# Optimization experiments

Measured on AMD Instinct MI355X. Metric: run time of the kernel, lower is better.

## Reference

```python
import jax, jax.numpy as jnp
import numpy as np


def setup_inputs() -> dict:
    key = jax.random.key(0)
    kq, kk, kv = jax.random.split(key, 3)
    B, S, D = 4, 4096, 128
    return {
        "q_proj": jax.random.normal(kq, (B, S, D), dtype=jnp.float32),
        "k_proj": jax.random.normal(kk, (B, S, D), dtype=jnp.float32),
        "v_proj": jax.random.normal(kv, (B, S, D), dtype=jnp.float32),
    }


def reference(q_proj, k_proj, v_proj):
    # Block-wise online softmax in the original is mathematically exact
    # full (non-causal) scaled dot-product attention.
    d = q_proj.shape[-1]
    scale = 1.0 / jnp.sqrt(jnp.asarray(d, dtype=q_proj.dtype))
    logits = jnp.einsum('bqd,bkd->bqk', q_proj, k_proj) * scale  # [B,S,S]
    attn = jax.nn.softmax(logits, axis=-1)
    return jnp.einsum('bqk,bkd->bqd', attn, v_proj)
```

## Files before the change

### kernel.cpp

```cpp
#include <hip/hip_runtime.h>
#include <hip/hip_bf16.h>
#include <stdint.h>

#define Bn 4
#define Sn 4096
#define Dn 128
#define SCALE ((float)(0.08838834764831843 * 1.4426950408889634))

typedef __attribute__((ext_vector_type(8)))  short short8;
typedef __attribute__((ext_vector_type(4)))  short short4v;
typedef __attribute__((ext_vector_type(4)))  float f32x4;
typedef __attribute__((ext_vector_type(16))) float f32x16;

__device__ __forceinline__ uint32_t bfround(float f){
  union { float f; uint32_t u; } a; a.f = f;
  return a.u + 0x7FFFu + ((a.u >> 16) & 1u);
}
__device__ __forceinline__ uint32_t f2bf2(float lo, float hi){
  return (bfround(hi) & 0xFFFF0000u) | (bfround(lo) >> 16);
}
__device__ __forceinline__ uint32_t f2bf2_fast(float lo, float hi){
  const uint32_t a = __float_as_uint(lo) + 0x8000u;
  const uint32_t b = __float_as_uint(hi) + 0x8000u;
  return __builtin_amdgcn_perm(b, a, 0x07060302u);
}
__device__ __forceinline__ float bf2f(short s){
  union { uint32_t u; float f; } a; a.u = ((uint32_t)(unsigned short)s) << 16; return a.f;
}
__device__ __forceinline__ float fexp2(float x){
#if __has_builtin(__builtin_amdgcn_exp2f)
  return __builtin_amdgcn_exp2f(x);
#else
  return exp2f(x);
#endif
}
__device__ __forceinline__ int bitswap23(int x){
  return (x & ~15) | ((x & 3) | (((x>>2)&1)<<3) | (((x>>3)&1)<<2));
}

__global__ void prep_kernel(const float* __restrict__ k, const float* __restrict__ v,
                            short* __restrict__ kf, short* __restrict__ vf){
  const int bid = blockIdx.x;
  const int tid = threadIdx.x;
  if (bid < 512){
    const int b  = bid >> 7, kt = bid & 127;
#pragma unroll
    for (int i=0;i<2;++i){
      const int idx = i*256 + tid;
      const int t = idx >> 6, lane = idx & 63;
      const int ln = lane & 31, h5 = lane >> 5;
      const float* src = k + ((size_t)(b*Sn + kt*32 + ln))*Dn + t*16 + h5*8;
      const f32x4 a = *(const f32x4*)src;
      const f32x4 c = *(const f32x4*)(src + 4);
      union { uint32_t u[4]; short8 s; } pk;
      pk.u[0] = f2bf2(a[0], a[1]);
      pk.u[1] = f2bf2(a[2], a[3]);
      pk.u[2] = f2bf2(c[0], c[1]);
      pk.u[3] = f2bf2(c[2], c[3]);
      *(short8*)(kf + ((((size_t)(b*128 + kt))*8 + t)*64 + lane)*8) = pk.s;
    }
  } else {
    __shared__ float tile[64][65];
    const int vb  = bid - 512;
    const int b   = vb >> 7;
    const int rem = vb & 127;
    const int s0t = rem & 63;
    const int d0t = rem >> 6;
    const int s0 = s0t*64, d0 = d0t*64;
#pragma unroll
    for (int i=0;i<16;++i){
      int lin = i*256 + tid;
      int r = lin >> 6, c = lin & 63;
      tile[r][c] = v[((size_t)(b*Sn + s0 + r))*Dn + d0 + c];
    }
    __syncthreads();
#pragma unroll
    for (int i=0;i<2;++i){
      const int idx = i*256 + tid;
      const int g = idx >> 6, lane = idx & 63;
      const int ln = lane & 31, h5 = lane >> 5;
      const int kt_l = g >> 2, t = (g >> 1) & 1, mt_l = g & 1;
      const int kt = s0t*2 + kt_l;
      const int mt = d0t*2 + mt_l;
      const int c  = 2*t + h5;
      const int dl = mt_l*32 + ln;
      union { uint32_t u[4]; short8 s; } pk;
#pragma unroll
      for (int p=0;p<2;++p){
        const int x0 = c*8 + 2*p*2;
      }
#pragma unroll
      for (int p=0;p<4;++p){
        const int x0 = c*8 + 2*p, x1 = x0 + 1;
        const int k0 = kt_l*32 + bitswap23(x0);
        const int k1 = kt_l*32 + bitswap23(x1);
        pk.u[p] = f2bf2(tile[k0][dl], tile[k1][dl]);
      }
      *(short8*)(vf + ((((size_t)(b*128 + kt))*8 + t*4 + mt)*64 + lane)*8) = pk.s;
    }
  }
}

__global__ __launch_bounds__(256, 3) void fa_kernel(
    const float* __restrict__ Qg, const short* __restrict__ KF,
    const short* __restrict__ VF, short* __restrict__ parts,
    float* __restrict__ lparts){
  const int tid = threadIdx.x;
  const int w = tid >> 6, lane = tid & 63;
  const int ln = lane & 31, h5 = lane >> 5;
  const int idx = blockIdx.x;
  const int b     = idx & 3;
  const int khalf = (idx >> 2) & 1;
  const int r     = idx >> 3;
  const int qt    = r & 31;
  const int kk    = r >> 5;
  const int ksIdx = khalf*3 + kk;
  const int q0    = qt * 128;
  const int start_kt = khalf*64 + (kk == 0 ? 0 : 22 + 21*(kk-1));
  const int n_it     = (kk == 0 ? 22 : 21);

  short8 Qf[8];
  {
    const float* qp = Qg + ((size_t)(b*Sn + q0 + w*32 + ln))*Dn;
#pragma unroll
    for (int t=0;t<8;++t){
      const int d0 = t*16 + h5*8;
      const f32x4 a = *(const f32x4*)(qp + d0);
      const f32x4 c = *(const f32x4*)(qp + d0 + 4);
      union { uint32_t u[4]; short8 s; } pk;
      pk.u[0] = f2bf2(a[0]*SCALE, a[1]*SCALE);
      pk.u[1] = f2bf2(a[2]*SCALE, a[3]*SCALE);
      pk.u[2] = f2bf2(c[0]*SCALE, c[1]*SCALE);
      pk.u[3] = f2bf2(c[2]*SCALE, c[3]*SCALE);
      Qf[t] = pk.s;
    }
  }

  f32x16 Ot[4];
#pragma unroll
  for (int m=0;m<4;++m)
#pragma unroll
    for (int rr=0;rr<16;++rr) Ot[m][rr] = 0.0f;
  float ls0=0.f, ls1=0.f, ls2=0.f, ls3=0.f;

  const short* kfp = KF + (((size_t)(b*128 + start_kt))*8)*512 + (size_t)lane*8;
  const short* vfp = VF + (((size_t)(b*128 + start_kt))*8)*512 + (size_t)lane*8;

  for (int i=0; i<n_it; ++i){
    short8 kf[8];
#pragma unroll
    for (int t=0;t<8;++t) kf[t] = *(const short8*)(kfp + (size_t)t*512);
    f32x16 St;
#pragma unroll
    for (int rr=0;rr<16;++rr) St[rr] = 0.0f;
#pragma unroll
    for (int t=0;t<8;++t)
      St = __builtin_amdgcn_mfma_f32_32x32x16_bf16(kf[t], Qf[t], St, 0, 0, 0);

    short8 vfr[8];
#pragma unroll
    for (int u=0;u<8;++u) vfr[u] = *(const short8*)(vfp + (size_t)u*512);

#pragma unroll
    for (int rr=0;rr<16;++rr) St[rr] = fexp2(St[rr]);
#pragma unroll
    for (int rr=0;rr<16;rr+=4){
      ls0 += St[rr]; ls1 += St[rr+1]; ls2 += St[rr+2]; ls3 += St[rr+3];
    }

#pragma unroll
    for (int t=0;t<2;++t){
      union { uint32_t u[4]; short8 s; } pf;
      pf.u[0] = f2bf2_fast(St[8*t+0], St[8*t+1]);
      pf.u[1] = f2bf2_fast(St[8*t+2], St[8*t+3]);
      pf.u[2] = f2bf2_fast(St[8*t+4], St[8*t+5]);
      pf.u[3] = f2bf2_fast(St[8*t+6], St[8*t+7]);
#pragma unroll
      for (int mt=0;mt<4;++mt)
        Ot[mt] = __builtin_amdgcn_mfma_f32_32x32x16_bf16(vfr[t*4+mt], pf.s, Ot[mt], 0, 0, 0);
    }

    kfp += 8*512;
    vfp += 8*512;
  }

  float lsum = (ls0 + ls1) + (ls2 + ls3);
  lsum += __shfl_xor(lsum, 32, 64);

  const int pslot = (b*32 + qt)*6 + ksIdx;
  short* pbase = parts + (size_t)pslot*16384 + (size_t)(w*32 + ln)*128;
#pragma unroll
  for (int mt=0;mt<4;++mt){
#pragma unroll
    for (int g=0;g<4;++g){
      union { uint32_t u[2]; short4v s; } o;
      o.u[0] = f2bf2(Ot[mt][4*g],   Ot[mt][4*g+1]);
      o.u[1] = f2bf2(Ot[mt][4*g+2], Ot[mt][4*g+3]);
      *(short4v*)(pbase + mt*32 + 8*g + 4*h5) = o.s;
    }
  }
  if (h5 == 0) lparts[(size_t)pslot*128 + w*32 + ln] = lsum;
}

__global__ void reduce_kernel(const short* __restrict__ parts,
                              const float* __restrict__ lparts,
                              float* __restrict__ out){
  const int t  = threadIdx.x;
  const int s  = blockIdx.x >> 3;
  const int qg = (blockIdx.x & 7)*16 + (t >> 4);
  const int d0 = (t & 15) * 8;
  float acc[8];
#pragma unroll
  for (int j=0;j<8;++j) acc[j] = 0.0f;
  float lsum = 0.0f;
#pragma unroll
  for (int ks=0;ks<6;++ks){
    const short8 p = *(const short8*)(parts + ((size_t)(s*6+ks))*16384 + (size_t)qg*128 + d0);
#pragma unroll
    for (int j=0;j<8;++j) acc[j] += bf2f(p[j]);
    lsum += lparts[(size_t)(s*6+ks)*128 + qg];
  }
  const float linv = 1.0f / lsum;
  f32x4 o0, o1;
#pragma unroll
  for (int j=0;j<4;++j){ o0[j] = acc[j]*linv; o1[j] = acc[4+j]*linv; }
  float* op = out + ((size_t)(s*128 + qg))*128 + d0;
  *(f32x4*)op = o0;
  *(f32x4*)(op + 4) = o1;
}

extern "C" void kernel_launch(void* const* d_in, const int* in_sizes, int n_in,
                              void* d_out, int out_size, void* d_ws, size_t ws_size,
                              hipStream_t stream){
  const float* q = (const float*)d_in[0];
  const float* k = (const float*)d_in[1];
  const float* v = (const float*)d_in[2];
  float* out = (float*)d_out;
  char* ws = (char*)d_ws;
  short* kfb    = (short*)ws;
  short* vfb    = kfb + (size_t)Bn*Sn*Dn;
  short* parts  = (short*)(ws + 8388608);
  float* lparts = (float*)(ws + 8388608 + 25165824);

  prep_kernel<<<1024, 256, 0, stream>>>(k, v, kfb, vfb);
  fa_kernel<<<768, 256, 0, stream>>>(q, kfb, vfb, parts, lparts);
  reduce_kernel<<<1024, 256, 0, stream>>>(parts, lparts, out);
}
```

Measured before the change: 128.4 us.

## Process two query tiles per wave with Q staged in LDS

Each wave now handles 64 query rows (two 32-row MFMA tiles) against every loaded K/V fragment, so each K/V register load feeds twice as much MFMA work. Q fragments are staged in 64KB of shared memory instead of registers to make room for the doubled accumulators. The key split changes from 6 to 8 chunks of 16 tiles, with 512 blocks and launch bounds reduced to 2 waves per SIMD. The reduce kernel and workspace layout are updated for 8 partials. This raises register and LDS pressure and lowers occupancy, and it adds partial-sum traffic.

```diff
diff --git a/kernel.cpp b/kernel.cpp
--- a/kernel.cpp
+++ b/kernel.cpp
@@ -86,10 +86,6 @@
       const int dl = mt_l*32 + ln;
       union { uint32_t u[4]; short8 s; } pk;
 #pragma unroll
-      for (int p=0;p<2;++p){
-        const int x0 = c*8 + 2*p*2;
-      }
-#pragma unroll
       for (int p=0;p<4;++p){
         const int x0 = c*8 + 2*p, x1 = x0 + 1;
         const int k0 = kt_l*32 + bitswap23(x0);
@@ -101,105 +97,133 @@
   }
 }
 
-__global__ __launch_bounds__(256, 3) void fa_kernel(
+__global__ __launch_bounds__(256, 2) void fa_kernel(
     const float* __restrict__ Qg, const short* __restrict__ KF,
     const short* __restrict__ VF, short* __restrict__ parts,
     float* __restrict__ lparts){
+  __shared__ __align__(16) char lds[65536];
   const int tid = threadIdx.x;
   const int w = tid >> 6, lane = tid & 63;
   const int ln = lane & 31, h5 = lane >> 5;
   const int idx = blockIdx.x;
   const int b     = idx & 3;
   const int khalf = (idx >> 2) & 1;
-  const int r     = idx >> 3;
-  const int qt    = r & 31;
-  const int kk    = r >> 5;
-  const int ksIdx = khalf*3 + kk;
-  const int q0    = qt * 128;
-  const int start_kt = khalf*64 + (kk == 0 ? 0 : 22 + 21*(kk-1));
-  const int n_it     = (kk == 0 ? 22 : 21);
-
-  short8 Qf[8];
-  {
-    const float* qp = Qg + ((size_t)(b*Sn + q0 + w*32 + ln))*Dn;
+  const int rest  = idx >> 3;
+  const int qblk  = rest & 15;
+  const int kk    = rest >> 4;
+  const int ksIdx = khalf*4 + kk;
+  const int start_kt = khalf*64 + kk*16;
+  const int qw0 = qblk*256 + w*64;
+
+  char* const ldsQ = lds + w*16384;
+
+#pragma unroll
+  for (int s=0;s<2;++s){
+    const float* qp = Qg + ((size_t)(b*Sn + qw0 + s*32 + ln))*Dn;
 #pragma unroll
     for (int t=0;t<8;++t){
       const int d0 = t*16 + h5*8;
       const f32x4 a = *(const f32x4*)(qp + d0);
       const f32x4 c = *(const f32x4*)(qp + d0 + 4);
-      union { uint32_t u[4]; short8 s; } pk;
+      union { uint32_t u[4]; short8 s8; } pk;
       pk.u[0] = f2bf2(a[0]*SCALE, a[1]*SCALE);
       pk.u[1] = f2bf2(a[2]*SCALE, a[3]*SCALE);
       pk.u[2] = f2bf2(c[0]*SCALE, c[1]*SCALE);
       pk.u[3] = f2bf2(c[2]*SCALE, c[3]*SCALE);
-      Qf[t] = pk.s;
-    }
-  }
-
-  f32x16 Ot[4];
+      *(short8*)(ldsQ + (s*8+t)*1024 + lane*16) = pk.s8;
+    }
+  }
+
+  f32x16 Oa[4], Ob[4];
 #pragma unroll
   for (int m=0;m<4;++m)
 #pragma unroll
-    for (int rr=0;rr<16;++rr) Ot[m][rr] = 0.0f;
-  float ls0=0.f, ls1=0.f, ls2=0.f, ls3=0.f;
+    for (int r=0;r<16;++r){ Oa[m][r] = 0.0f; Ob[m][r] = 0.0f; }
+  float la0=0.f, la1=0.f, la2=0.f, la3=0.f;
+  float lb0=0.f, lb1=0.f, lb2=0.f, lb3=0.f;
 
   const short* kfp = KF + (((size_t)(b*128 + start_kt))*8)*512 + (size_t)lane*8;
   const short* vfp = VF + (((size_t)(b*128 + start_kt))*8)*512 + (size_t)lane*8;
 
-  for (int i=0; i<n_it; ++i){
+  for (int i=0; i<16; ++i){
     short8 kf[8];
 #pragma unroll
     for (int t=0;t<8;++t) kf[t] = *(const short8*)(kfp + (size_t)t*512);
-    f32x16 St;
-#pragma unroll
-    for (int rr=0;rr<16;++rr) St[rr] = 0.0f;
-#pragma unroll
-    for (int t=0;t<8;++t)
-      St = __builtin_amdgcn_mfma_f32_32x32x16_bf16(kf[t], Qf[t], St, 0, 0, 0);
-
-    short8 vfr[8];
-#pragma unroll
-    for (int u=0;u<8;++u) vfr[u] = *(const short8*)(vfp + (size_t)u*512);
-
-#pragma unroll
-    for (int rr=0;rr<16;++rr) St[rr] = fexp2(St[rr]);
-#pragma unroll
-    for (int rr=0;rr<16;rr+=4){
-      ls0 += St[rr]; ls1 += St[rr+1]; ls2 += St[rr+2]; ls3 += St[rr+3];
+
+    f32x16 Sa, Sb;
+#pragma unroll
+    for (int r=0;r<16;++r){ Sa[r]=0.0f; Sb[r]=0.0f; }
+#pragma unroll
+    for (int t=0;t<8;++t){
+      const short8 qa = *(const short8*)(ldsQ + t*1024 + lane*16);
+      const short8 qb = *(const short8*)(ldsQ + 8192 + t*1024 + lane*16);
+      Sa = __builtin_amdgcn_mfma_f32_32x32x16_bf16(kf[t], qa, Sa, 0, 0, 0);
+      Sb = __builtin_amdgcn_mfma_f32_32x32x16_bf16(kf[t], qb, Sb, 0, 0, 0);
+    }
+
+    short8 vf[8];
+#pragma unroll
+    for (int u=0;u<8;++u) vf[u] = *(const short8*)(vfp + (size_t)u*512);
+
+#pragma unroll
+    for (int r=0;r<16;++r) Sa[r] = fexp2(Sa[r]);
+#pragma unroll
+    for (int r=0;r<16;++r) Sb[r] = fexp2(Sb[r]);
+#pragma unroll
+    for (int r=0;r<16;r+=4){
+      la0 += Sa[r]; la1 += Sa[r+1]; la2 += Sa[r+2]; la3 += Sa[r+3];
+      lb0 += Sb[r]; lb1 += Sb[r+1]; lb2 += Sb[r+2]; lb3 += Sb[r+3];
     }
 
 #pragma unroll
     for (int t=0;t<2;++t){
-      union { uint32_t u[4]; short8 s; } pf;
-      pf.u[0] = f2bf2_fast(St[8*t+0], St[8*t+1]);
-      pf.u[1] = f2bf2_fast(St[8*t+2], St[8*t+3]);
-      pf.u[2] = f2bf2_fast(St[8*t+4], St[8*t+5]);
-      pf.u[3] = f2bf2_fast(St[8*t+6], St[8*t+7]);
-#pragma unroll
-      for (int mt=0;mt<4;++mt)
-        Ot[mt] = __builtin_amdgcn_mfma_f32_32x32x16_bf16(vfr[t*4+mt], pf.s, Ot[mt], 0, 0, 0);
+      union { uint32_t u[4]; short8 s; } pa, pb;
+      pa.u[0] = f2bf2_fast(Sa[8*t+0], Sa[8*t+1]);
+      pa.u[1] = f2bf2_fast(Sa[8*t+2], Sa[8*t+3]);
+      pa.u[2] = f2bf2_fast(Sa[8*t+4], Sa[8*t+5]);
+      pa.u[3] = f2bf2_fast(Sa[8*t+6], Sa[8*t+7]);
+      pb.u[0] = f2bf2_fast(Sb[8*t+0], Sb[8*t+1]);
+      pb.u[1] = f2bf2_fast(Sb[8*t+2], Sb[8*t+3]);
+      pb.u[2] = f2bf2_fast(Sb[8*t+4], Sb[8*t+5]);
+      pb.u[3] = f2bf2_fast(Sb[8*t+6], Sb[8*t+7]);
+#pragma unroll
+      for (int mt=0;mt<4;++mt){
+        Oa[mt] = __builtin_amdgcn_mfma_f32_32x32x16_bf16(vf[t*4+mt], pa.s, Oa[mt], 0, 0, 0);
+        Ob[mt] = __builtin_amdgcn_mfma_f32_32x32x16_bf16(vf[t*4+mt], pb.s, Ob[mt], 0, 0, 0);
+      }
     }
 
     kfp += 8*512;
     vfp += 8*512;
   }
 
-  float lsum = (ls0 + ls1) + (ls2 + ls3);
-  lsum += __shfl_xor(lsum, 32, 64);
-
-  const int pslot = (b*32 + qt)*6 + ksIdx;
-  short* pbase = parts + (size_t)pslot*16384 + (size_t)(w*32 + ln)*128;
+  float lsa = (la0 + la1) + (la2 + la3);
+  float lsb = (lb0 + lb1) + (lb2 + lb3);
+  lsa += __shfl_xor(lsa, 32, 64);
+  lsb += __shfl_xor(lsb, 32, 64);
+
+  const int qt128 = qblk*2 + (w >> 1);
+  const int pslot = (b*32 + qt128)*8 + ksIdx;
+  const int rbase = (w & 1)*64;
+  short* pb0 = parts + (size_t)pslot*16384 + (size_t)(rbase + ln)*128;
+  short* pb1 = parts + (size_t)pslot*16384 + (size_t)(rbase + 32 + ln)*128;
 #pragma unroll
   for (int mt=0;mt<4;++mt){
 #pragma unroll
     for (int g=0;g<4;++g){
-      union { uint32_t u[2]; short4v s; } o;
-      o.u[0] = f2bf2(Ot[mt][4*g],   Ot[mt][4*g+1]);
-      o.u[1] = f2bf2(Ot[mt][4*g+2], Ot[mt][4*g+3]);
-      *(short4v*)(pbase + mt*32 + 8*g + 4*h5) = o.s;
-    }
-  }
-  if (h5 == 0) lparts[(size_t)pslot*128 + w*32 + ln] = lsum;
+      union { uint32_t u[2]; short4v s; } oa, ob;
+      oa.u[0] = f2bf2(Oa[mt][4*g],   Oa[mt][4*g+1]);
+      oa.u[1] = f2bf2(Oa[mt][4*g+2], Oa[mt][4*g+3]);
+      ob.u[0] = f2bf2(Ob[mt][4*g],   Ob[mt][4*g+1]);
+      ob.u[1] = f2bf2(Ob[mt][4*g+2], Ob[mt][4*g+3]);
+      *(short4v*)(pb0 + mt*32 + 8*g + 4*h5) = oa.s;
+      *(short4v*)(pb1 + mt*32 + 8*g + 4*h5) = ob.s;
+    }
+  }
+  if (h5 == 0){
+    lparts[(size_t)pslot*128 + rbase + ln]      = lsa;
+    lparts[(size_t)pslot*128 + rbase + 32 + ln] = lsb;
+  }
 }
 
 __global__ void reduce_kernel(const short* __restrict__ parts,
@@ -214,11 +238,11 @@
   for (int j=0;j<8;++j) acc[j] = 0.0f;
   float lsum = 0.0f;
 #pragma unroll
-  for (int ks=0;ks<6;++ks){
-    const short8 p = *(const short8*)(parts + ((size_t)(s*6+ks))*16384 + (size_t)qg*128 + d0);
+  for (int ks=0;ks<8;++ks){
+    const short8 p = *(const short8*)(parts + ((size_t)(s*8+ks))*16384 + (size_t)qg*128 + d0);
 #pragma unroll
     for (int j=0;j<8;++j) acc[j] += bf2f(p[j]);
-    lsum += lparts[(size_t)(s*6+ks)*128 + qg];
+    lsum += lparts[(size_t)(s*8+ks)*128 + qg];
   }
   const float linv = 1.0f / lsum;
   f32x4 o0, o1;
@@ -240,9 +264,9 @@
   short* kfb    = (short*)ws;
   short* vfb    = kfb + (size_t)Bn*Sn*Dn;
   short* parts  = (short*)(ws + 8388608);
-  float* lparts = (float*)(ws + 8388608 + 25165824);
+  float* lparts = (float*)(ws + 8388608 + 33554432);
 
   prep_kernel<<<1024, 256, 0, stream>>>(k, v, kfb, vfb);
-  fa_kernel<<<768, 256, 0, stream>>>(q, kfb, vfb, parts, lparts);
+  fa_kernel<<<512, 256, 0, stream>>>(q, kfb, vfb, parts, lparts);
   reduce_kernel<<<1024, 256, 0, stream>>>(parts, lparts, out);
 }
```

Result: slower. 162.6 us (+26.6%).

## Split keys four ways, stage Q in LDS, double-buffer K fragment loads

Applied to the files above, without the earlier changes.

Changes the key split from six uneven chunks to four 32-tile chunks, so the grid drops from 768 to 512 blocks and the reduce kernel sums four partials instead of six. Q fragments move from registers to per-wave LDS and are re-read for every tile. The K loads for the next tile are issued a tile ahead through two alternating register buffers, and the V loads are split into two halves. Occupancy falls from 3 to 2 blocks per CU, and fewer blocks with longer loops may leave CUs idle or cut latency hiding, in exchange for more load/compute overlap and less reduction traffic.

```diff
diff --git a/kernel.cpp b/kernel.cpp
--- a/kernel.cpp
+++ b/kernel.cpp
@@ -86,10 +86,6 @@
       const int dl = mt_l*32 + ln;
       union { uint32_t u[4]; short8 s; } pk;
 #pragma unroll
-      for (int p=0;p<2;++p){
-        const int x0 = c*8 + 2*p*2;
-      }
-#pragma unroll
       for (int p=0;p<4;++p){
         const int x0 = c*8 + 2*p, x1 = x0 + 1;
         const int k0 = kt_l*32 + bitswap23(x0);
@@ -101,25 +97,25 @@
   }
 }
 
-__global__ __launch_bounds__(256, 3) void fa_kernel(
+__global__ __launch_bounds__(256, 2) void fa_kernel(
     const float* __restrict__ Qg, const short* __restrict__ KF,
     const short* __restrict__ VF, short* __restrict__ parts,
     float* __restrict__ lparts){
+  __shared__ __align__(16) char lds[32768];
   const int tid = threadIdx.x;
   const int w = tid >> 6, lane = tid & 63;
   const int ln = lane & 31, h5 = lane >> 5;
   const int idx = blockIdx.x;
   const int b     = idx & 3;
   const int khalf = (idx >> 2) & 1;
-  const int r     = idx >> 3;
-  const int qt    = r & 31;
-  const int kk    = r >> 5;
-  const int ksIdx = khalf*3 + kk;
-  const int q0    = qt * 128;
-  const int start_kt = khalf*64 + (kk == 0 ? 0 : 22 + 21*(kk-1));
-  const int n_it     = (kk == 0 ? 22 : 21);
-
-  short8 Qf[8];
+  const int kk    = (idx >> 3) & 1;
+  const int qt    = idx >> 4;
+  const int ksIdx = khalf*2 + kk;
+  const int start_kt = ksIdx * 32;
+  const int q0 = qt * 128;
+
+  char* const ldsQ = lds + w*8192;
+
   {
     const float* qp = Qg + ((size_t)(b*Sn + q0 + w*32 + ln))*Dn;
 #pragma unroll
@@ -127,12 +123,12 @@
       const int d0 = t*16 + h5*8;
       const f32x4 a = *(const f32x4*)(qp + d0);
       const f32x4 c = *(const f32x4*)(qp + d0 + 4);
-      union { uint32_t u[4]; short8 s; } pk;
+      union { uint32_t u[4]; short8 s8; } pk;
       pk.u[0] = f2bf2(a[0]*SCALE, a[1]*SCALE);
       pk.u[1] = f2bf2(a[2]*SCALE, a[3]*SCALE);
       pk.u[2] = f2bf2(c[0]*SCALE, c[1]*SCALE);
       pk.u[3] = f2bf2(c[2]*SCALE, c[3]*SCALE);
-      Qf[t] = pk.s;
+      *(short8*)(ldsQ + t*1024 + lane*16) = pk.s8;
     }
   }
 
@@ -140,54 +136,74 @@
 #pragma unroll
   for (int m=0;m<4;++m)
 #pragma unroll
-    for (int rr=0;rr<16;++rr) Ot[m][rr] = 0.0f;
+    for (int r=0;r<16;++r) Ot[m][r] = 0.0f;
   float ls0=0.f, ls1=0.f, ls2=0.f, ls3=0.f;
 
   const short* kfp = KF + (((size_t)(b*128 + start_kt))*8)*512 + (size_t)lane*8;
   const short* vfp = VF + (((size_t)(b*128 + start_kt))*8)*512 + (size_t)lane*8;
 
-  for (int i=0; i<n_it; ++i){
-    short8 kf[8];
-#pragma unroll
-    for (int t=0;t<8;++t) kf[t] = *(const short8*)(kfp + (size_t)t*512);
+  short8 kA[8], kB[8];
+#pragma unroll
+  for (int t=0;t<8;++t) kA[t] = *(const short8*)(kfp + (size_t)t*512);
+  kfp += 4096;
+
+  auto body = [&](short8* kc, short8* kn, int i){
+    if (i < 31){
+#pragma unroll
+      for (int t=0;t<8;++t) kn[t] = *(const short8*)(kfp + (size_t)t*512);
+      kfp += 4096;
+    }
+    short8 v0[4];
+#pragma unroll
+    for (int u=0;u<4;++u) v0[u] = *(const short8*)(vfp + (size_t)u*512);
+
     f32x16 St;
 #pragma unroll
-    for (int rr=0;rr<16;++rr) St[rr] = 0.0f;
-#pragma unroll
-    for (int t=0;t<8;++t)
-      St = __builtin_amdgcn_mfma_f32_32x32x16_bf16(kf[t], Qf[t], St, 0, 0, 0);
-
-    short8 vfr[8];
-#pragma unroll
-    for (int u=0;u<8;++u) vfr[u] = *(const short8*)(vfp + (size_t)u*512);
-
-#pragma unroll
-    for (int rr=0;rr<16;++rr) St[rr] = fexp2(St[rr]);
-#pragma unroll
-    for (int rr=0;rr<16;rr+=4){
-      ls0 += St[rr]; ls1 += St[rr+1]; ls2 += St[rr+2]; ls3 += St[rr+3];
-    }
-
-#pragma unroll
-    for (int t=0;t<2;++t){
-      union { uint32_t u[4]; short8 s; } pf;
-      pf.u[0] = f2bf2_fast(St[8*t+0], St[8*t+1]);
-      pf.u[1] = f2bf2_fast(St[8*t+2], St[8*t+3]);
-      pf.u[2] = f2bf2_fast(St[8*t+4], St[8*t+5]);
-      pf.u[3] = f2bf2_fast(St[8*t+6], St[8*t+7]);
-#pragma unroll
-      for (int mt=0;mt<4;++mt)
-        Ot[mt] = __builtin_amdgcn_mfma_f32_32x32x16_bf16(vfr[t*4+mt], pf.s, Ot[mt], 0, 0, 0);
-    }
-
-    kfp += 8*512;
-    vfp += 8*512;
+    for (int r=0;r<16;++r) St[r] = 0.0f;
+#pragma unroll
+    for (int t=0;t<8;++t){
+      const short8 qa = *(const short8*)(ldsQ + t*1024 + lane*16);
+      St = __builtin_amdgcn_mfma_f32_32x32x16_bf16(kc[t], qa, St, 0, 0, 0);
+    }
+
+    short8 v1[4];
+#pragma unroll
+    for (int u=0;u<4;++u) v1[u] = *(const short8*)(vfp + (size_t)(4+u)*512);
+    vfp += 4096;
+
+#pragma unroll
+    for (int r=0;r<16;++r) St[r] = fexp2(St[r]);
+#pragma unroll
+    for (int r=0;r<16;r+=4){
+      ls0 += St[r]; ls1 += St[r+1]; ls2 += St[r+2]; ls3 += St[r+3];
+    }
+
+    union { uint32_t u[4]; short8 s; } p0, p1;
+    p0.u[0] = f2bf2_fast(St[0],  St[1]);
+    p0.u[1] = f2bf2_fast(St[2],  St[3]);
+    p0.u[2] = f2bf2_fast(St[4],  St[5]);
+    p0.u[3] = f2bf2_fast(St[6],  St[7]);
+    p1.u[0] = f2bf2_fast(St[8],  St[9]);
+    p1.u[1] = f2bf2_fast(St[10], St[11]);
+    p1.u[2] = f2bf2_fast(St[12], St[13]);
+    p1.u[3] = f2bf2_fast(St[14], St[15]);
+#pragma unroll
+    for (int mt=0;mt<4;++mt)
+      Ot[mt] = __builtin_amdgcn_mfma_f32_32x32x16_bf16(v0[mt], p0.s, Ot[mt], 0, 0, 0);
+#pragma unroll
+    for (int mt=0;mt<4;++mt)
+      Ot[mt] = __builtin_amdgcn_mfma_f32_32x32x16_bf16(v1[mt], p1.s, Ot[mt], 0, 0, 0);
+  };
+
+  for (int i=0; i<32; i+=2){
+    body(kA, kB, i);
+    body(kB, kA, i+1);
   }
 
   float lsum = (ls0 + ls1) + (ls2 + ls3);
   lsum += __shfl_xor(lsum, 32, 64);
 
-  const int pslot = (b*32 + qt)*6 + ksIdx;
+  const int pslot = (b*32 + qt)*4 + ksIdx;
   short* pbase = parts + (size_t)pslot*16384 + (size_t)(w*32 + ln)*128;
 #pragma unroll
   for (int mt=0;mt<4;++mt){
@@ -214,11 +230,11 @@
   for (int j=0;j<8;++j) acc[j] = 0.0f;
   float lsum = 0.0f;
 #pragma unroll
-  for (int ks=0;ks<6;++ks){
-    const short8 p = *(const short8*)(parts + ((size_t)(s*6+ks))*16384 + (size_t)qg*128 + d0);
+  for (int ks=0;ks<4;++ks){
+    const short8 p = *(const short8*)(parts + ((size_t)(s*4+ks))*16384 + (size_t)qg*128 + d0);
 #pragma unroll
     for (int j=0;j<8;++j) acc[j] += bf2f(p[j]);
-    lsum += lparts[(size_t)(s*6+ks)*128 + qg];
+    lsum += lparts[(size_t)(s*4+ks)*128 + qg];
   }
   const float linv = 1.0f / lsum;
   f32x4 o0, o1;
@@ -240,9 +256,9 @@
   short* kfb    = (short*)ws;
   short* vfb    = kfb + (size_t)Bn*Sn*Dn;
   short* parts  = (short*)(ws + 8388608);
-  float* lparts = (float*)(ws + 8388608 + 25165824);
+  float* lparts = (float*)(ws + 8388608 + 16777216);
 
   prep_kernel<<<1024, 256, 0, stream>>>(k, v, kfb, vfb);
-  fa_kernel<<<768, 256, 0, stream>>>(q, kfb, vfb, parts, lparts);
+  fa_kernel<<<512, 256, 0, stream>>>(q, kfb, vfb, parts, lparts);
   reduce_kernel<<<1024, 256, 0, stream>>>(parts, lparts, out);
 }
```

Measured after the change: 123.5 us. 3.9% less time.
